# Performance work log

Hardware: AMD Instinct MI355X
Metric: run time of the kernel (lower is better)

The kernel has to match this reference:

```python
import jax, jax.numpy as jnp
import numpy as np
import math

N_EMBED = 768
N_HEAD = 12
BLOCK_SIZE = 2048
B, T = 4, 2048


def setup_inputs() -> dict:
    key = jax.random.key(0)
    ks = jax.random.split(key, 5)
    x = jax.random.normal(ks[0], (B, T, N_EMBED), dtype=jnp.float32)
    # attn: Linear(n_embed, 3*n_embed); torch Linear stores W as [out,in]
    s = 1.0 / math.sqrt(N_EMBED)
    W_attn = jax.random.uniform(ks[1], (3 * N_EMBED, N_EMBED), minval=-s, maxval=s, dtype=jnp.float32)
    b_attn = jax.random.uniform(ks[2], (3 * N_EMBED,), minval=-s, maxval=s, dtype=jnp.float32)
    W_o = jax.random.uniform(ks[3], (N_EMBED, N_EMBED), minval=-s, maxval=s, dtype=jnp.float32)
    b_o = jax.random.uniform(ks[4], (N_EMBED,), minval=-s, maxval=s, dtype=jnp.float32)
    return {"x": x, "W_attn": W_attn, "b_attn": b_attn, "W_o": W_o, "b_o": b_o}


def reference(x, W_attn, b_attn, W_o, b_o):
    Bsz, Tlen, C = x.shape
    hd = C // N_HEAD
    qkv = x @ W_attn.T + b_attn                       # [B,T,3C]
    q, k, v = jnp.split(qkv, 3, axis=2)
    # [B,H,T,hd]
    q = q.reshape(Bsz, Tlen, N_HEAD, hd).transpose(0, 2, 1, 3)
    k = k.reshape(Bsz, Tlen, N_HEAD, hd).transpose(0, 2, 1, 3)
    v = v.reshape(Bsz, Tlen, N_HEAD, hd).transpose(0, 2, 1, 3)
    att = jnp.einsum('bhqd,bhkd->bhqk', q, k) * (1.0 / math.sqrt(hd))
    causal = jnp.tril(jnp.ones((Tlen, Tlen), dtype=bool))
    att = jnp.where(causal[None, None], att, -jnp.inf)
    att = jax.nn.softmax(att, axis=-1)
    y = jnp.einsum('bhqk,bhkd->bhqd', att, v)          # [B,H,T,hd]
    y = y.transpose(0, 2, 1, 3).reshape(Bsz, Tlen, C)
    return y @ W_o.T + b_o
```

## Files before the change

kernel.cpp:

```cpp
#include <hip/hip_runtime.h>

#define H 12
#define T 2048
#define HD 64
#define CEMB 768
#define M1 8192
#define N1 2304
#define K1 768

typedef __attribute__((ext_vector_type(8))) short bf8;
typedef __attribute__((ext_vector_type(4))) float f4;
typedef __attribute__((ext_vector_type(16))) float f16v;
typedef __attribute__((ext_vector_type(4))) int i4;

__device__ __forceinline__ unsigned short f2bf(float f){
  union { float f; unsigned u; } v; v.f = f;
  unsigned r = v.u + 0x7FFFu + ((v.u >> 16) & 1u);
  return (unsigned short)(r >> 16);
}

__device__ __forceinline__ int cvtpk(float a, float b){
  int r;
  asm("v_cvt_pk_bf16_f32 %0, %1, %2" : "=v"(r) : "v"(a), "v"(b));
  return r;
}

__device__ __forceinline__ void gload16(const unsigned short* g, unsigned short* l){
  __builtin_amdgcn_global_load_lds((const __attribute__((address_space(1))) void*)g,
                                   (__attribute__((address_space(3))) void*)l, 16, 0, 0);
}

__global__ __launch_bounds__(256) void cvt_f32_bf16(const float* __restrict__ in,
                                                    unsigned short* __restrict__ out, int n4){
  int i = blockIdx.x * blockDim.x + threadIdx.x;
  if (i < n4){
    float4 v = ((const float4*)in)[i];
    ushort4 o;
    o.x = f2bf(v.x); o.y = f2bf(v.y); o.z = f2bf(v.z); o.w = f2bf(v.w);
    ((ushort4*)out)[i] = o;
  }
}

__global__ __launch_bounds__(256) void gemm_qkv(const unsigned short* __restrict__ A,
                                                const unsigned short* __restrict__ Wb,
                                                const float* __restrict__ bias,
                                                unsigned short* __restrict__ Qb,
                                                unsigned short* __restrict__ Kb,
                                                unsigned short* __restrict__ Vr){
  __shared__ __align__(16) unsigned short As[128][64];
  __shared__ __align__(16) unsigned short Bs[128][64];
  int Lid = blockIdx.x + gridDim.x * blockIdx.y;
  int L2 = (Lid & 7) * 144 + (Lid >> 3);
  const int m0 = (L2 / 18) * 128, n0 = (L2 % 18) * 128;
  const int tid = threadIdx.x, w = tid >> 6, lane = tid & 63;
  const int wm = (w >> 1) * 64, wn = (w & 1) * 64;
  const int l15 = lane & 15, g = lane >> 4;
  const int srow = lane >> 3;
  const int scol = ((lane & 7) ^ srow) * 8;
  f4 acc[4][4] = {};
  for (int k0 = 0; k0 < K1; k0 += 64){
    #pragma unroll
    for (int i = 0; i < 4; ++i){
      int rb = i * 32 + w * 8;
      gload16(&A [(size_t)(m0 + rb + srow) * K1 + k0 + scol], &As[rb][0]);
      gload16(&Wb[(size_t)(n0 + rb + srow) * K1 + k0 + scol], &Bs[rb][0]);
    }
    __syncthreads();
    #pragma unroll
    for (int kq = 0; kq < 2; ++kq){
      bf8 a[4], b[4];
      #pragma unroll
      for (int i = 0; i < 4; ++i){
        int row = wm + i * 16 + l15;
        a[i] = *(const bf8*)&As[row][(((kq << 2) + g) ^ (row & 7)) * 8];
      }
      #pragma unroll
      for (int j = 0; j < 4; ++j){
        int row = wn + j * 16 + l15;
        b[j] = *(const bf8*)&Bs[row][(((kq << 2) + g) ^ (row & 7)) * 8];
      }
      #pragma unroll
      for (int i = 0; i < 4; ++i)
        #pragma unroll
        for (int j = 0; j < 4; ++j)
          acc[i][j] = __builtin_amdgcn_mfma_f32_16x16x32_bf16(a[i], b[j], acc[i][j], 0, 0, 0);
    }
    __syncthreads();
  }
  #pragma unroll
  for (int j = 0; j < 4; ++j){
    int ncol = n0 + wn + j * 16 + l15;
    float bv = bias[ncol];
    int which = ncol / CEMB;
    int cc = ncol - which * CEMB;
    int h = cc >> 6, d = cc & 63;
    #pragma unroll
    for (int i = 0; i < 4; ++i){
      #pragma unroll
      for (int r = 0; r < 4; ++r){
        int m = m0 + wm + i * 16 + g * 4 + r;
        int b_ = m >> 11, t = m & 2047;
        size_t idx = ((size_t)(b_ * H + h) * T + t) * HD + d;
        float v = acc[i][j][r] + bv;
        if (which == 0)      Qb[idx] = f2bf(v * 0.18033688f);
        else if (which == 1) Kb[idx] = f2bf(v);
        else                 Vr[idx] = f2bf(v);
      }
    }
  }
}

__global__ __launch_bounds__(256) void transpose_v(const unsigned short* __restrict__ Vr,
                                                   unsigned short* __restrict__ Vt){
  __shared__ unsigned short Lb[64][66];
  const int bh = blockIdx.y, tt = blockIdx.x;
  const unsigned short* src = Vr + ((size_t)bh * T + tt * 64) * HD;
  unsigned short* dst = Vt + (size_t)bh * HD * T + tt * 64;
  const int tid = threadIdx.x;
  {
    int r = tid >> 2, c = (tid & 3) * 16;
    uint4 v0 = *(const uint4*)&src[r * HD + c];
    uint4 v1 = *(const uint4*)&src[r * HD + c + 8];
    unsigned* lp = (unsigned*)&Lb[r][c];
    lp[0] = v0.x; lp[1] = v0.y; lp[2] = v0.z; lp[3] = v0.w;
    lp[4] = v1.x; lp[5] = v1.y; lp[6] = v1.z; lp[7] = v1.w;
  }
  __syncthreads();
  {
    int d = tid >> 2, tq = tid & 3;
    unsigned ov[8];
    #pragma unroll
    for (int jj = 0; jj < 8; ++jj){
      unsigned lo = Lb[tq * 16 + 2 * jj][d];
      unsigned hi = Lb[tq * 16 + 2 * jj + 1][d];
      ov[jj] = lo | (hi << 16);
    }
    uint4* op = (uint4*)&dst[(size_t)d * T + tq * 16];
    op[0] = make_uint4(ov[0], ov[1], ov[4], ov[5]);
    op[1] = make_uint4(ov[2], ov[3], ov[6], ov[7]);
  }
}

__global__ __launch_bounds__(64) void attn(const unsigned short* __restrict__ Qb,
                                           const unsigned short* __restrict__ Kb,
                                           const unsigned short* __restrict__ Vt,
                                           unsigned short* __restrict__ Yb){
  __shared__ __align__(16) unsigned short Ks[2][32][64];
  __shared__ __align__(16) unsigned short Vs[2][64][32];
  __shared__ float scb[32];
  const int bh = blockIdx.x;
  const int qidx = 63 - (int)blockIdx.y;
  const int lane = threadIdx.x;
  const int q31 = lane & 31, hi = lane >> 5;
  const int q0 = qidx * 32;
  const unsigned short* Qp = Qb + (size_t)bh * T * HD;
  const unsigned short* Kp = Kb + (size_t)bh * T * HD;
  const unsigned short* Vp = Vt + (size_t)bh * HD * T;
  const int b_ = bh / H, h = bh % H;

  const int krow = lane >> 3;
  const int kcs  = ((lane & 7) ^ krow) * 8;
  const int vrow = lane >> 2;
  const int vcs  = ((lane & 3) ^ (vrow & 3)) * 8;

  bf8 qf[4];
  #pragma unroll
  for (int ds = 0; ds < 4; ++ds)
    qf[ds] = *(const bf8*)&Qp[(q0 + q31) * HD + ds * 16 + hi * 8];

  f16v o0 = {}, o1 = {};
  float m_i = -1e30f, l_i = 0.f;
  const int ntw = qidx + 1;

  #pragma unroll
  for (int it = 0; it < 4; ++it)
    gload16(&Kp[(size_t)(it * 8 + krow) * HD + kcs], &Ks[0][it * 8][0]);
  #pragma unroll
  for (int it = 0; it < 4; ++it)
    gload16(&Vp[(size_t)(it * 16 + vrow) * T + vcs], &Vs[0][it * 16][0]);

  #pragma unroll 2
  for (int t = 0; t < ntw; ++t){
    const int cur = t & 1;
    const int kv0 = t * 32;
    if (t + 1 < ntw){
      const int nkv = kv0 + 32;
      #pragma unroll
      for (int it = 0; it < 4; ++it)
        gload16(&Kp[(size_t)(nkv + it * 8 + krow) * HD + kcs], &Ks[cur ^ 1][it * 8][0]);
      #pragma unroll
      for (int it = 0; it < 4; ++it)
        gload16(&Vp[(size_t)(it * 16 + vrow) * T + nkv + vcs], &Vs[cur ^ 1][it * 16][0]);
      asm volatile("s_waitcnt vmcnt(8)" ::: "memory");
    } else {
      asm volatile("s_waitcnt vmcnt(0)" ::: "memory");
    }
    __builtin_amdgcn_sched_barrier(0);

    f16v s0 = {};
    __builtin_amdgcn_s_setprio(1);
    #pragma unroll
    for (int ds = 0; ds < 4; ++ds){
      bf8 k0 = *(const bf8*)&Ks[cur][q31][(((2 * ds + hi)) ^ (q31 & 7)) * 8];
      s0 = __builtin_amdgcn_mfma_f32_32x32x16_bf16(k0, qf[ds], s0, 0, 0, 0);
    }
    __builtin_amdgcn_s_setprio(0);
    if (t == ntw - 1){
      #pragma unroll
      for (int r = 0; r < 16; ++r){
        int kvr = kv0 + (r & 3) + 8 * (r >> 2) + 4 * hi;
        if (kvr > q0 + q31) s0[r] = -1e30f;
      }
    }
    float tm[16];
    #pragma unroll
    for (int r = 0; r < 16; ++r) tm[r] = s0[r];
    #pragma unroll
    for (int st = 8; st > 0; st >>= 1)
      #pragma unroll
      for (int r = 0; r < 8; ++r) if (r < st) tm[r] = fmaxf(tm[r], tm[r + st]);
    float mx = fmaxf(tm[0], __shfl_xor(tm[0], 32));
    if (__any(mx > m_i + 8.f)){
      float mn = fmaxf(m_i, mx);
      float sc_ = __builtin_exp2f(m_i - mn);
      l_i *= sc_;
      scb[q31] = sc_;
      asm volatile("s_waitcnt lgkmcnt(0)" ::: "memory");
      __builtin_amdgcn_sched_barrier(0);
      #pragma unroll
      for (int j = 0; j < 4; ++j){
        float4 sq = *(const float4*)&scb[8 * j + 4 * hi];
        #pragma unroll
        for (int i = 0; i < 4; ++i){
          o0[4 * j + i] *= ((const float*)&sq)[i];
          o1[4 * j + i] *= ((const float*)&sq)[i];
        }
      }
      m_i = mn;
    }
    #pragma unroll
    for (int r = 0; r < 16; ++r) s0[r] = __builtin_exp2f(s0[r] - m_i);
    float ts[16];
    #pragma unroll
    for (int r = 0; r < 16; ++r) ts[r] = s0[r];
    #pragma unroll
    for (int st = 8; st > 0; st >>= 1)
      #pragma unroll
      for (int r = 0; r < 8; ++r) if (r < st) ts[r] += ts[r + st];
    l_i += ts[0] + __shfl_xor(ts[0], 32);
    union { i4 i; bf8 h; } pa;
    __builtin_amdgcn_s_setprio(1);
    #pragma unroll
    for (int ks = 0; ks < 2; ++ks){
      const int off = ks * 8;
      pa.i = (i4){ cvtpk(s0[off], s0[off+1]), cvtpk(s0[off+2], s0[off+3]),
                   cvtpk(s0[off+4], s0[off+5]), cvtpk(s0[off+6], s0[off+7]) };
      bf8 v0 = *(const bf8*)&Vs[cur][q31]     [((2 * ks + hi) ^ (q31 & 3)) * 8];
      bf8 v1 = *(const bf8*)&Vs[cur][32 + q31][((2 * ks + hi) ^ (q31 & 3)) * 8];
      o0 = __builtin_amdgcn_mfma_f32_32x32x16_bf16(pa.h, v0, o0, 0, 0, 0);
      o1 = __builtin_amdgcn_mfma_f32_32x32x16_bf16(pa.h, v1, o1, 0, 0, 0);
    }
    __builtin_amdgcn_s_setprio(0);
  }

  scb[q31] = 1.0f / l_i;
  asm volatile("s_waitcnt lgkmcnt(0)" ::: "memory");
  __builtin_amdgcn_sched_barrier(0);
  #pragma unroll
  for (int j = 0; j < 4; ++j){
    float4 sq = *(const float4*)&scb[8 * j + 4 * hi];
    #pragma unroll
    for (int i = 0; i < 4; ++i){
      int r = 4 * j + i;
      int qrow = q0 + (r & 3) + 8 * (r >> 2) + 4 * hi;
      float inv = ((const float*)&sq)[i];
      size_t base = ((size_t)b_ * T + qrow) * CEMB + h * HD;
      Yb[base + q31]      = f2bf(o0[r] * inv);
      Yb[base + 32 + q31] = f2bf(o1[r] * inv);
    }
  }
}

__global__ __launch_bounds__(256) void gemm_out(const unsigned short* __restrict__ A,
                                                const unsigned short* __restrict__ Wb,
                                                const float* __restrict__ bias,
                                                float* __restrict__ out){
  __shared__ __align__(16) unsigned short As[128][64];
  __shared__ __align__(16) unsigned short Bs[128][64];
  int Lid = blockIdx.x + gridDim.x * blockIdx.y;
  int L2 = (Lid & 7) * 48 + (Lid >> 3);
  const int m0 = (L2 / 6) * 128, n0 = (L2 % 6) * 128;
  const int tid = threadIdx.x, w = tid >> 6, lane = tid & 63;
  const int wm = (w >> 1) * 64, wn = (w & 1) * 64;
  const int l15 = lane & 15, g = lane >> 4;
  const int srow = lane >> 3;
  const int scol = ((lane & 7) ^ srow) * 8;
  f4 acc[4][4] = {};
  for (int k0 = 0; k0 < CEMB; k0 += 64){
    #pragma unroll
    for (int i = 0; i < 4; ++i){
      int rb = i * 32 + w * 8;
      gload16(&A [(size_t)(m0 + rb + srow) * CEMB + k0 + scol], &As[rb][0]);
      gload16(&Wb[(size_t)(n0 + rb + srow) * CEMB + k0 + scol], &Bs[rb][0]);
    }
    __syncthreads();
    #pragma unroll
    for (int kq = 0; kq < 2; ++kq){
      bf8 a[4], b[4];
      #pragma unroll
      for (int i = 0; i < 4; ++i){
        int row = wm + i * 16 + l15;
        a[i] = *(const bf8*)&As[row][(((kq << 2) + g) ^ (row & 7)) * 8];
      }
      #pragma unroll
      for (int j = 0; j < 4; ++j){
        int row = wn + j * 16 + l15;
        b[j] = *(const bf8*)&Bs[row][(((kq << 2) + g) ^ (row & 7)) * 8];
      }
      #pragma unroll
      for (int i = 0; i < 4; ++i)
        #pragma unroll
        for (int j = 0; j < 4; ++j)
          acc[i][j] = __builtin_amdgcn_mfma_f32_16x16x32_bf16(a[i], b[j], acc[i][j], 0, 0, 0);
    }
    __syncthreads();
  }
  #pragma unroll
  for (int j = 0; j < 4; ++j){
    int ncol = n0 + wn + j * 16 + l15;
    float bv = bias[ncol];
    #pragma unroll
    for (int i = 0; i < 4; ++i){
      #pragma unroll
      for (int r = 0; r < 4; ++r){
        int m = m0 + wm + i * 16 + g * 4 + r;
        out[(size_t)m * CEMB + ncol] = acc[i][j][r] + bv;
      }
    }
  }
}

extern "C" void kernel_launch(void* const* d_in, const int* in_sizes, int n_in,
                              void* d_out, int out_size, void* d_ws, size_t ws_size,
                              hipStream_t stream){
  const float* x      = (const float*)d_in[0];
  const float* W_attn = (const float*)d_in[1];
  const float* b_attn = (const float*)d_in[2];
  const float* W_o    = (const float*)d_in[3];
  const float* b_o    = (const float*)d_in[4];
  float* out = (float*)d_out;

  char* ws = (char*)d_ws;
  const size_t SZ_T  = (size_t)48 * T * HD * 2;
  const size_t SZ_WA = (size_t)N1 * K1 * 2;
  const size_t SZ_WO = (size_t)CEMB * CEMB * 2;
  unsigned short* Xb = (unsigned short*)(ws);
  unsigned short* Vt = (unsigned short*)(ws);
  unsigned short* Wa = (unsigned short*)(ws + SZ_T);
  unsigned short* Wo = (unsigned short*)(ws + SZ_T + SZ_WA);
  unsigned short* Qb = (unsigned short*)(ws + SZ_T + SZ_WA + SZ_WO);
  unsigned short* Kb = (unsigned short*)(ws + SZ_T + SZ_WA + SZ_WO + SZ_T);
  unsigned short* Vr = (unsigned short*)(ws + SZ_T + SZ_WA + SZ_WO + 2 * SZ_T);
  unsigned short* Yb = Vr;

  cvt_f32_bf16<<<(M1 * K1 / 4 + 255) / 256, 256, 0, stream>>>(x, Xb, M1 * K1 / 4);
  cvt_f32_bf16<<<(N1 * K1 / 4 + 255) / 256, 256, 0, stream>>>(W_attn, Wa, N1 * K1 / 4);
  cvt_f32_bf16<<<(CEMB * CEMB / 4 + 255) / 256, 256, 0, stream>>>(W_o, Wo, CEMB * CEMB / 4);

  gemm_qkv<<<dim3(N1 / 128, M1 / 128), 256, 0, stream>>>(Xb, Wa, b_attn, Qb, Kb, Vr);
  transpose_v<<<dim3(T / 64, 48), 256, 0, stream>>>(Vr, Vt);
  attn<<<dim3(48, 64), 64, 0, stream>>>(Qb, Kb, Vt, Yb);
  gemm_out<<<dim3(CEMB / 128, M1 / 128), 256, 0, stream>>>(Yb, Wo, b_o, out);
}
```

Measured before the change: 173.9 us.

## Load K/V fragments directly into registers with ping-pong prefetch instead of LDS

The attention kernel stops staging K and V tiles through double-buffered shared memory. Each lane now loads its MFMA operand fragments straight from global memory into two register sets, prefetching the next tile while the current one is computed. This removes the LDS writes and reads and their waitcnt stalls, and launch bounds now request 3 waves per SIMD. In exchange, every lane issues strided 16-byte global loads, V loads are scattered across rows, register pressure rises, and there is no explicit wait, so latency hiding depends on the compiler's scheduling.

```diff
diff --git a/kernel.cpp b/kernel.cpp
--- a/kernel.cpp
+++ b/kernel.cpp
@@ -141,12 +141,90 @@
   }
 }
 
-__global__ __launch_bounds__(64) void attn(const unsigned short* __restrict__ Qb,
-                                           const unsigned short* __restrict__ Kb,
-                                           const unsigned short* __restrict__ Vt,
-                                           unsigned short* __restrict__ Yb){
-  __shared__ __align__(16) unsigned short Ks[2][32][64];
-  __shared__ __align__(16) unsigned short Vs[2][64][32];
+__device__ __forceinline__ void attn_stage(const unsigned short* __restrict__ Kp,
+                                           const unsigned short* __restrict__ Vp,
+                                           bf8 (&kf)[4], bf8 (&vf)[4],
+                                           int kv0, int q31, int hi){
+  #pragma unroll
+  for (int ds = 0; ds < 4; ++ds)
+    kf[ds] = *(const bf8*)&Kp[(size_t)(kv0 + q31) * HD + (2 * ds + hi) * 8];
+  #pragma unroll
+  for (int ks = 0; ks < 2; ++ks){
+    vf[2 * ks]     = *(const bf8*)&Vp[(size_t)q31 * T        + kv0 + (2 * ks + hi) * 8];
+    vf[2 * ks + 1] = *(const bf8*)&Vp[(size_t)(32 + q31) * T + kv0 + (2 * ks + hi) * 8];
+  }
+}
+
+__device__ __forceinline__ void attn_tile(const bf8 (&kf)[4], const bf8 (&vf)[4],
+                                          const bf8 (&qf)[4], f16v& o0, f16v& o1,
+                                          float& m_i, float& l_i, float* scb,
+                                          int kv0, bool diag, int q0, int q31, int hi){
+  f16v s0 = {};
+  __builtin_amdgcn_s_setprio(1);
+  #pragma unroll
+  for (int ds = 0; ds < 4; ++ds)
+    s0 = __builtin_amdgcn_mfma_f32_32x32x16_bf16(kf[ds], qf[ds], s0, 0, 0, 0);
+  __builtin_amdgcn_s_setprio(0);
+  if (diag){
+    #pragma unroll
+    for (int r = 0; r < 16; ++r){
+      int kvr = kv0 + (r & 3) + 8 * (r >> 2) + 4 * hi;
+      if (kvr > q0 + q31) s0[r] = -1e30f;
+    }
+  }
+  float tm[16];
+  #pragma unroll
+  for (int r = 0; r < 16; ++r) tm[r] = s0[r];
+  #pragma unroll
+  for (int st = 8; st > 0; st >>= 1)
+    #pragma unroll
+    for (int r = 0; r < 8; ++r) if (r < st) tm[r] = fmaxf(tm[r], tm[r + st]);
+  float mx = fmaxf(tm[0], __shfl_xor(tm[0], 32));
+  if (__any(mx > m_i + 8.f)){
+    float mn = fmaxf(m_i, mx);
+    float sc_ = __builtin_exp2f(m_i - mn);
+    l_i *= sc_;
+    scb[q31] = sc_;
+    asm volatile("s_waitcnt lgkmcnt(0)" ::: "memory");
+    __builtin_amdgcn_sched_barrier(0);
+    #pragma unroll
+    for (int j = 0; j < 4; ++j){
+      float4 sq = *(const float4*)&scb[8 * j + 4 * hi];
+      #pragma unroll
+      for (int i = 0; i < 4; ++i){
+        o0[4 * j + i] *= ((const float*)&sq)[i];
+        o1[4 * j + i] *= ((const float*)&sq)[i];
+      }
+    }
+    m_i = mn;
+  }
+  #pragma unroll
+  for (int r = 0; r < 16; ++r) s0[r] = __builtin_exp2f(s0[r] - m_i);
+  float ts[16];
+  #pragma unroll
+  for (int r = 0; r < 16; ++r) ts[r] = s0[r];
+  #pragma unroll
+  for (int st = 8; st > 0; st >>= 1)
+    #pragma unroll
+    for (int r = 0; r < 8; ++r) if (r < st) ts[r] += ts[r + st];
+  l_i += ts[0] + __shfl_xor(ts[0], 32);
+  union { i4 i; bf8 h; } pa;
+  __builtin_amdgcn_s_setprio(1);
+  #pragma unroll
+  for (int ks = 0; ks < 2; ++ks){
+    const int off = ks * 8;
+    pa.i = (i4){ cvtpk(s0[off], s0[off+1]), cvtpk(s0[off+2], s0[off+3]),
+                 cvtpk(s0[off+4], s0[off+5]), cvtpk(s0[off+6], s0[off+7]) };
+    o0 = __builtin_amdgcn_mfma_f32_32x32x16_bf16(pa.h, vf[2 * ks],     o0, 0, 0, 0);
+    o1 = __builtin_amdgcn_mfma_f32_32x32x16_bf16(pa.h, vf[2 * ks + 1], o1, 0, 0, 0);
+  }
+  __builtin_amdgcn_s_setprio(0);
+}
+
+__global__ __launch_bounds__(64, 3) void attn(const unsigned short* __restrict__ Qb,
+                                              const unsigned short* __restrict__ Kb,
+                                              const unsigned short* __restrict__ Vt,
+                                              unsigned short* __restrict__ Yb){
   __shared__ float scb[32];
   const int bh = blockIdx.x;
   const int qidx = 63 - (int)blockIdx.y;
@@ -158,11 +236,6 @@
   const unsigned short* Vp = Vt + (size_t)bh * HD * T;
   const int b_ = bh / H, h = bh % H;
 
-  const int krow = lane >> 3;
-  const int kcs  = ((lane & 7) ^ krow) * 8;
-  const int vrow = lane >> 2;
-  const int vcs  = ((lane & 3) ^ (vrow & 3)) * 8;
-
   bf8 qf[4];
   #pragma unroll
   for (int ds = 0; ds < 4; ++ds)
@@ -172,95 +245,17 @@
   float m_i = -1e30f, l_i = 0.f;
   const int ntw = qidx + 1;
 
-  #pragma unroll
-  for (int it = 0; it < 4; ++it)
-    gload16(&Kp[(size_t)(it * 8 + krow) * HD + kcs], &Ks[0][it * 8][0]);
-  #pragma unroll
-  for (int it = 0; it < 4; ++it)
-    gload16(&Vp[(size_t)(it * 16 + vrow) * T + vcs], &Vs[0][it * 16][0]);
-
-  #pragma unroll 2
-  for (int t = 0; t < ntw; ++t){
-    const int cur = t & 1;
-    const int kv0 = t * 32;
-    if (t + 1 < ntw){
-      const int nkv = kv0 + 32;
-      #pragma unroll
-      for (int it = 0; it < 4; ++it)
-        gload16(&Kp[(size_t)(nkv + it * 8 + krow) * HD + kcs], &Ks[cur ^ 1][it * 8][0]);
-      #pragma unroll
-      for (int it = 0; it < 4; ++it)
-        gload16(&Vp[(size_t)(it * 16 + vrow) * T + nkv + vcs], &Vs[cur ^ 1][it * 16][0]);
-      asm volatile("s_waitcnt vmcnt(8)" ::: "memory");
-    } else {
-      asm volatile("s_waitcnt vmcnt(0)" ::: "memory");
-    }
-    __builtin_amdgcn_sched_barrier(0);
-
-    f16v s0 = {};
-    __builtin_amdgcn_s_setprio(1);
-    #pragma unroll
-    for (int ds = 0; ds < 4; ++ds){
-      bf8 k0 = *(const bf8*)&Ks[cur][q31][(((2 * ds + hi)) ^ (q31 & 7)) * 8];
-      s0 = __builtin_amdgcn_mfma_f32_32x32x16_bf16(k0, qf[ds], s0, 0, 0, 0);
-    }
-    __builtin_amdgcn_s_setprio(0);
-    if (t == ntw - 1){
-      #pragma unroll
-      for (int r = 0; r < 16; ++r){
-        int kvr = kv0 + (r & 3) + 8 * (r >> 2) + 4 * hi;
-        if (kvr > q0 + q31) s0[r] = -1e30f;
-      }
-    }
-    float tm[16];
-    #pragma unroll
-    for (int r = 0; r < 16; ++r) tm[r] = s0[r];
-    #pragma unroll
-    for (int st = 8; st > 0; st >>= 1)
-      #pragma unroll
-      for (int r = 0; r < 8; ++r) if (r < st) tm[r] = fmaxf(tm[r], tm[r + st]);
-    float mx = fmaxf(tm[0], __shfl_xor(tm[0], 32));
-    if (__any(mx > m_i + 8.f)){
-      float mn = fmaxf(m_i, mx);
-      float sc_ = __builtin_exp2f(m_i - mn);
-      l_i *= sc_;
-      scb[q31] = sc_;
-      asm volatile("s_waitcnt lgkmcnt(0)" ::: "memory");
-      __builtin_amdgcn_sched_barrier(0);
-      #pragma unroll
-      for (int j = 0; j < 4; ++j){
-        float4 sq = *(const float4*)&scb[8 * j + 4 * hi];
-        #pragma unroll
-        for (int i = 0; i < 4; ++i){
-          o0[4 * j + i] *= ((const float*)&sq)[i];
-          o1[4 * j + i] *= ((const float*)&sq)[i];
-        }
-      }
-      m_i = mn;
-    }
-    #pragma unroll
-    for (int r = 0; r < 16; ++r) s0[r] = __builtin_exp2f(s0[r] - m_i);
-    float ts[16];
-    #pragma unroll
-    for (int r = 0; r < 16; ++r) ts[r] = s0[r];
-    #pragma unroll
-    for (int st = 8; st > 0; st >>= 1)
-      #pragma unroll
-      for (int r = 0; r < 8; ++r) if (r < st) ts[r] += ts[r + st];
-    l_i += ts[0] + __shfl_xor(ts[0], 32);
-    union { i4 i; bf8 h; } pa;
-    __builtin_amdgcn_s_setprio(1);
-    #pragma unroll
-    for (int ks = 0; ks < 2; ++ks){
-      const int off = ks * 8;
-      pa.i = (i4){ cvtpk(s0[off], s0[off+1]), cvtpk(s0[off+2], s0[off+3]),
-                   cvtpk(s0[off+4], s0[off+5]), cvtpk(s0[off+6], s0[off+7]) };
-      bf8 v0 = *(const bf8*)&Vs[cur][q31]     [((2 * ks + hi) ^ (q31 & 3)) * 8];
-      bf8 v1 = *(const bf8*)&Vs[cur][32 + q31][((2 * ks + hi) ^ (q31 & 3)) * 8];
-      o0 = __builtin_amdgcn_mfma_f32_32x32x16_bf16(pa.h, v0, o0, 0, 0, 0);
-      o1 = __builtin_amdgcn_mfma_f32_32x32x16_bf16(pa.h, v1, o1, 0, 0, 0);
-    }
-    __builtin_amdgcn_s_setprio(0);
+  bf8 kfA[4], vfA[4], kfB[4], vfB[4];
+  attn_stage(Kp, Vp, kfA, vfA, 0, q31, hi);
+
+  int t = 0;
+  for (;;){
+    if (t + 1 < ntw) attn_stage(Kp, Vp, kfB, vfB, (t + 1) * 32, q31, hi);
+    attn_tile(kfA, vfA, qf, o0, o1, m_i, l_i, scb, t * 32, t == ntw - 1, q0, q31, hi);
+    if (++t >= ntw) break;
+    if (t + 1 < ntw) attn_stage(Kp, Vp, kfA, vfA, (t + 1) * 32, q31, hi);
+    attn_tile(kfB, vfB, qf, o0, o1, m_i, l_i, scb, t * 32, t == ntw - 1, q0, q31, hi);
+    if (++t >= ntw) break;
   }
 
   scb[q31] = 1.0f / l_i;
```

Measured after the change: 202.3 us. 16.4% more time.

## Split long causal attention query tiles into two KV halves with a merge kernel

Applied to the files above, without the earlier changes.

Query tiles in the upper half of the sequence now have their KV range split across two workgroups, so each workgroup writes unnormalized partial outputs plus running max and sum to a workspace. A new merge kernel combines the two partials with softmax rescaling and writes bf16 output. This is meant to shorten the longest workgroups and balance load across the causal triangle, at the cost of an extra launch and fp32 partial traffic. The V shared-memory swizzle pattern is also changed, likely to reduce bank conflicts.

```diff
diff --git a/kernel.cpp b/kernel.cpp
--- a/kernel.cpp
+++ b/kernel.cpp
@@ -144,15 +144,24 @@
 __global__ __launch_bounds__(64) void attn(const unsigned short* __restrict__ Qb,
                                            const unsigned short* __restrict__ Kb,
                                            const unsigned short* __restrict__ Vt,
-                                           unsigned short* __restrict__ Yb){
+                                           unsigned short* __restrict__ Yb,
+                                           float* __restrict__ P_O,
+                                           float* __restrict__ P_ml){
   __shared__ __align__(16) unsigned short Ks[2][32][64];
   __shared__ __align__(16) unsigned short Vs[2][64][32];
   __shared__ float scb[32];
   const int bh = blockIdx.x;
-  const int qidx = 63 - (int)blockIdx.y;
+  const int by = blockIdx.y;
+  int q, t0, t1, part;
+  if (by < 32){ q = 31 - by; part = -1; t0 = 0; t1 = q + 1; }
+  else {
+    int i = (by - 32) >> 1; q = 63 - i; part = (by - 32) & 1;
+    int n = q + 1, hh = n >> 1;
+    t0 = part ? hh : 0; t1 = part ? n : hh;
+  }
   const int lane = threadIdx.x;
   const int q31 = lane & 31, hi = lane >> 5;
-  const int q0 = qidx * 32;
+  const int q0 = q * 32;
   const unsigned short* Qp = Qb + (size_t)bh * T * HD;
   const unsigned short* Kp = Kb + (size_t)bh * T * HD;
   const unsigned short* Vp = Vt + (size_t)bh * HD * T;
@@ -161,7 +170,7 @@
   const int krow = lane >> 3;
   const int kcs  = ((lane & 7) ^ krow) * 8;
   const int vrow = lane >> 2;
-  const int vcs  = ((lane & 3) ^ (vrow & 3)) * 8;
+  const int vcs  = ((lane & 3) ^ ((lane >> 4) & 3)) * 8;
 
   bf8 qf[4];
   #pragma unroll
@@ -170,20 +179,22 @@
 
   f16v o0 = {}, o1 = {};
   float m_i = -1e30f, l_i = 0.f;
-  const int ntw = qidx + 1;
-
-  #pragma unroll
-  for (int it = 0; it < 4; ++it)
-    gload16(&Kp[(size_t)(it * 8 + krow) * HD + kcs], &Ks[0][it * 8][0]);
-  #pragma unroll
-  for (int it = 0; it < 4; ++it)
-    gload16(&Vp[(size_t)(it * 16 + vrow) * T + vcs], &Vs[0][it * 16][0]);
+
+  {
+    const int kv0 = t0 * 32;
+    #pragma unroll
+    for (int it = 0; it < 4; ++it)
+      gload16(&Kp[(size_t)(kv0 + it * 8 + krow) * HD + kcs], &Ks[0][it * 8][0]);
+    #pragma unroll
+    for (int it = 0; it < 4; ++it)
+      gload16(&Vp[(size_t)(it * 16 + vrow) * T + kv0 + vcs], &Vs[0][it * 16][0]);
+  }
 
   #pragma unroll 2
-  for (int t = 0; t < ntw; ++t){
-    const int cur = t & 1;
+  for (int t = t0; t < t1; ++t){
+    const int cur = (t - t0) & 1;
     const int kv0 = t * 32;
-    if (t + 1 < ntw){
+    if (t + 1 < t1){
       const int nkv = kv0 + 32;
       #pragma unroll
       for (int it = 0; it < 4; ++it)
@@ -205,7 +216,7 @@
       s0 = __builtin_amdgcn_mfma_f32_32x32x16_bf16(k0, qf[ds], s0, 0, 0, 0);
     }
     __builtin_amdgcn_s_setprio(0);
-    if (t == ntw - 1){
+    if (t == q){
       #pragma unroll
       for (int r = 0; r < 16; ++r){
         int kvr = kv0 + (r & 3) + 8 * (r >> 2) + 4 * hi;
@@ -255,29 +266,75 @@
       const int off = ks * 8;
       pa.i = (i4){ cvtpk(s0[off], s0[off+1]), cvtpk(s0[off+2], s0[off+3]),
                    cvtpk(s0[off+4], s0[off+5]), cvtpk(s0[off+6], s0[off+7]) };
-      bf8 v0 = *(const bf8*)&Vs[cur][q31]     [((2 * ks + hi) ^ (q31 & 3)) * 8];
-      bf8 v1 = *(const bf8*)&Vs[cur][32 + q31][((2 * ks + hi) ^ (q31 & 3)) * 8];
+      bf8 v0 = *(const bf8*)&Vs[cur][q31]     [((2 * ks + hi) ^ ((q31 >> 2) & 3)) * 8];
+      bf8 v1 = *(const bf8*)&Vs[cur][32 + q31][((2 * ks + hi) ^ ((q31 >> 2) & 3)) * 8];
       o0 = __builtin_amdgcn_mfma_f32_32x32x16_bf16(pa.h, v0, o0, 0, 0, 0);
       o1 = __builtin_amdgcn_mfma_f32_32x32x16_bf16(pa.h, v1, o1, 0, 0, 0);
     }
     __builtin_amdgcn_s_setprio(0);
   }
 
-  scb[q31] = 1.0f / l_i;
-  asm volatile("s_waitcnt lgkmcnt(0)" ::: "memory");
-  __builtin_amdgcn_sched_barrier(0);
+  if (part < 0){
+    scb[q31] = 1.0f / l_i;
+    asm volatile("s_waitcnt lgkmcnt(0)" ::: "memory");
+    __builtin_amdgcn_sched_barrier(0);
+    #pragma unroll
+    for (int j = 0; j < 4; ++j){
+      float4 sq = *(const float4*)&scb[8 * j + 4 * hi];
+      #pragma unroll
+      for (int i = 0; i < 4; ++i){
+        int r = 4 * j + i;
+        int qrow = q0 + (r & 3) + 8 * (r >> 2) + 4 * hi;
+        float inv = ((const float*)&sq)[i];
+        size_t base = ((size_t)b_ * T + qrow) * CEMB + h * HD;
+        Yb[base + q31]      = f2bf(o0[r] * inv);
+        Yb[base + 32 + q31] = f2bf(o1[r] * inv);
+      }
+    }
+  } else {
+    const int qt = q - 32;
+    float* Pml = P_ml + (((size_t)(bh * 32 + qt) * 2 + part) * 2) * 32;
+    if (hi == 0){ Pml[q31] = m_i; Pml[32 + q31] = l_i; }
+    float* Po = P_O + (((size_t)(bh * 32 + qt) * 2 + part) * 32) * 64;
+    #pragma unroll
+    for (int r = 0; r < 16; ++r){
+      int row = (r & 3) + 8 * (r >> 2) + 4 * hi;
+      Po[row * 64 + q31]      = o0[r];
+      Po[row * 64 + 32 + q31] = o1[r];
+    }
+  }
+}
+
+__global__ __launch_bounds__(256) void merge_attn(const float* __restrict__ P_O,
+                                                  const float* __restrict__ P_ml,
+                                                  unsigned short* __restrict__ Yb){
+  const int bh = blockIdx.y, qt = blockIdx.x;
+  const int b_ = bh / H, h = bh % H;
+  const int tid = threadIdx.x;
+  const int row = tid >> 3, d0 = (tid & 7) * 8;
+  const size_t basml = ((size_t)(bh * 32 + qt) * 2) * 2 * 32;
+  float m0 = P_ml[basml + row];
+  float l0 = P_ml[basml + 32 + row];
+  float m1 = P_ml[basml + 64 + row];
+  float l1 = P_ml[basml + 96 + row];
+  float M = fmaxf(m0, m1);
+  float w0 = __builtin_exp2f(m0 - M), w1 = __builtin_exp2f(m1 - M);
+  float inv = 1.0f / (l0 * w0 + l1 * w1);
+  const size_t baso = ((size_t)(bh * 32 + qt) * 2) * 32 * 64;
+  const float* O0 = P_O + baso + row * 64 + d0;
+  const float* O1 = P_O + baso + 2048 + row * 64 + d0;
+  int qrow = (32 + qt) * 32 + row;
+  unsigned short* Y = Yb + ((size_t)b_ * T + qrow) * CEMB + h * HD + d0;
   #pragma unroll
-  for (int j = 0; j < 4; ++j){
-    float4 sq = *(const float4*)&scb[8 * j + 4 * hi];
-    #pragma unroll
-    for (int i = 0; i < 4; ++i){
-      int r = 4 * j + i;
-      int qrow = q0 + (r & 3) + 8 * (r >> 2) + 4 * hi;
-      float inv = ((const float*)&sq)[i];
-      size_t base = ((size_t)b_ * T + qrow) * CEMB + h * HD;
-      Yb[base + q31]      = f2bf(o0[r] * inv);
-      Yb[base + 32 + q31] = f2bf(o1[r] * inv);
-    }
+  for (int j = 0; j < 2; ++j){
+    float4 a = *(const float4*)&O0[4 * j];
+    float4 b = *(const float4*)&O1[4 * j];
+    ushort4 o;
+    o.x = f2bf((a.x * w0 + b.x * w1) * inv);
+    o.y = f2bf((a.y * w0 + b.y * w1) * inv);
+    o.z = f2bf((a.z * w0 + b.z * w1) * inv);
+    o.w = f2bf((a.w * w0 + b.w * w1) * inv);
+    ((ushort4*)Y)[j] = o;
   }
 }
 
@@ -362,6 +419,10 @@
   unsigned short* Kb = (unsigned short*)(ws + SZ_T + SZ_WA + SZ_WO + SZ_T);
   unsigned short* Vr = (unsigned short*)(ws + SZ_T + SZ_WA + SZ_WO + 2 * SZ_T);
   unsigned short* Yb = Vr;
+  const size_t off_p = 4 * SZ_T + SZ_WA + SZ_WO;
+  const size_t SZ_PO = (size_t)48 * 32 * 2 * 32 * 64 * 4;
+  float* P_O  = (float*)(ws + off_p);
+  float* P_ml = (float*)(ws + off_p + SZ_PO);
 
   cvt_f32_bf16<<<(M1 * K1 / 4 + 255) / 256, 256, 0, stream>>>(x, Xb, M1 * K1 / 4);
   cvt_f32_bf16<<<(N1 * K1 / 4 + 255) / 256, 256, 0, stream>>>(W_attn, Wa, N1 * K1 / 4);
@@ -369,6 +430,7 @@
 
   gemm_qkv<<<dim3(N1 / 128, M1 / 128), 256, 0, stream>>>(Xb, Wa, b_attn, Qb, Kb, Vr);
   transpose_v<<<dim3(T / 64, 48), 256, 0, stream>>>(Vr, Vt);
-  attn<<<dim3(48, 64), 64, 0, stream>>>(Qb, Kb, Vt, Yb);
+  attn<<<dim3(48, 96), 64, 0, stream>>>(Qb, Kb, Vt, Yb, P_O, P_ml);
+  merge_attn<<<dim3(32, 48), 256, 0, stream>>>(P_O, P_ml, Yb);
   gemm_out<<<dim3(CEMB / 128, M1 / 128), 256, 0, stream>>>(Yb, Wo, b_o, out);
 }
```

New measurement: 176.2 us. No clear change (+1.3%).
